# Performance work log

Hardware: AMD Instinct MI355X
Metric: run time of the kernel (lower is better)

Reference implementation:

```python
import jax, jax.numpy as jnp
import numpy as np

CUTOFF_UPPER = 4.5
EYE3 = jnp.eye(3, dtype=jnp.float32)


def tensor_norm(t):
    return (t ** 2).sum((-2, -1))


def decompose_tensor(X):
    # X: [N, C, 3, 3]
    tr_mean = jnp.trace(X, axis1=-2, axis2=-1) / 3.0
    I = tr_mean[..., None, None] * EYE3
    Xt = jnp.swapaxes(X, -2, -1)
    A = 0.5 * (X - Xt)
    S = 0.5 * (X + Xt) - I
    return I, A, S


def chan_linear(T, W, b):
    # torch: Linear applied over the channel axis after permute(0,2,3,1)
    # T: [N, C, 3, 3], W: [C, C], b: [C]
    return jnp.einsum('nkij,ck->ncij', T, W) + b[None, :, None, None]


def setup_inputs() -> dict:
    key = jax.random.key(0)
    ks = jax.random.split(key, 16)
    Np1, H, R, E = 20001, 128, 64, 200000
    X = jax.random.normal(ks[0], (Np1, H, 3, 3), dtype=jnp.float32)
    edge_index = jax.random.randint(ks[1], (2, E), 0, Np1)
    edge_weight = jax.random.uniform(ks[2], (E,), dtype=jnp.float32) * CUTOFF_UPPER
    edge_attr = jax.random.normal(ks[3], (E, R), dtype=jnp.float32)
    s = lambda fin: 1.0 / np.sqrt(fin)
    W1 = jax.random.uniform(ks[4], (3, H, H), minval=-s(H), maxval=s(H), dtype=jnp.float32)
    b1 = jax.random.uniform(ks[5], (3, H), minval=-s(H), maxval=s(H), dtype=jnp.float32)
    W2a = jax.random.uniform(ks[6], (H, R), minval=-s(R), maxval=s(R), dtype=jnp.float32)
    b2a = jax.random.uniform(ks[7], (H,), minval=-s(R), maxval=s(R), dtype=jnp.float32)
    W2b = jax.random.uniform(ks[8], (2 * H, H), minval=-s(H), maxval=s(H), dtype=jnp.float32)
    b2b = jax.random.uniform(ks[9], (2 * H,), minval=-s(H), maxval=s(H), dtype=jnp.float32)
    W2c = jax.random.uniform(ks[10], (3 * H, 2 * H), minval=-s(2 * H), maxval=s(2 * H), dtype=jnp.float32)
    b2c = jax.random.uniform(ks[11], (3 * H,), minval=-s(2 * H), maxval=s(2 * H), dtype=jnp.float32)
    W3 = jax.random.uniform(ks[12], (3, H, H), minval=-s(H), maxval=s(H), dtype=jnp.float32)
    b3 = jax.random.uniform(ks[13], (3, H), minval=-s(H), maxval=s(H), dtype=jnp.float32)
    return dict(X=X, edge_index=edge_index, edge_weight=edge_weight, edge_attr=edge_attr,
                W1=W1, b1=b1, W2a=W2a, b2a=b2a, W2b=W2b, b2b=b2b, W2c=W2c, b2c=b2c, W3=W3, b3=b3)


def reference(X, edge_index, edge_weight, edge_attr, W1, b1, W2a, b2a, W2b, b2b, W2c, b2c, W3, b3):
    Np1, H = X.shape[0], X.shape[1]
    act = jax.nn.silu
    X = X / (tensor_norm(X) + 1.0)[..., None, None]
    I, A, S = decompose_tensor(X)
    I = chan_linear(I, W1[0], b1[0])
    A = chan_linear(A, W1[1], b1[1])
    S = chan_linear(S, W1[2], b1[2])
    Y = I + A + S
    h = act(edge_attr @ W2a.T + b2a)
    h = act(h @ W2b.T + b2b)
    h = act(h @ W2c.T + b2c)  # [E, 3H]
    C = 0.5 * (jnp.cos(edge_weight * (jnp.pi / CUTOFF_UPPER)) + 1.0)
    C = C * (edge_weight < CUTOFF_UPPER).astype(C.dtype)
    ea = (h * C[:, None]).reshape(h.shape[0], H, 3)
    dst, src = edge_index[0], edge_index[1]

    def mp(factor, T):
        msg = factor[:, :, None, None] * T[src]  # [E, H, 3, 3]
        return jax.ops.segment_sum(msg, dst, num_segments=Np1)

    msg = mp(ea[..., 0], I) + mp(ea[..., 1], A) + mp(ea[..., 2], S)
    new_features = jnp.matmul(msg, Y) + jnp.matmul(Y, msg)  # O(3) branch
    I, A, S = decompose_tensor(new_features)
    norm = (tensor_norm(I + A + S) + 1.0)[..., None, None]
    I, A, S = I / norm, A / norm, S / norm
    I = chan_linear(I, W3[0], b3[0])
    A = chan_linear(A, W3[1], b3[1])
    S = chan_linear(S, W3[2], b3[2])
    dX = I + A + S
    return X + dX + jnp.matmul(dX, dX)
```

## Files before the change

kernel.cpp:

```cpp
#include <hip/hip_runtime.h>
#include <math.h>
#include <stdint.h>

typedef unsigned short u16;
typedef __attribute__((ext_vector_type(8))) short short8;
typedef __attribute__((ext_vector_type(4))) float floatx4;

__device__ __forceinline__ float b2f(u16 u){
  union{unsigned int i; float f;} v; v.i = ((unsigned int)u)<<16; return v.f;
}
__device__ __forceinline__ u16 f2b(float f){
  union{unsigned int i; float f;} v; v.f = f;
  unsigned int r = (v.i + 0x7FFFu + ((v.i>>16)&1u))>>16;
  return (u16)r;
}
__device__ __forceinline__ unsigned int pu(u16 lo, u16 hi){
  return (unsigned int)lo | ((unsigned int)hi<<16);
}
__device__ __forceinline__ float gsel(unsigned int u, int s){
  return b2f((u16)(s ? (u>>16) : (u & 0xffffu)));
}
__device__ __forceinline__ unsigned int cvtpk(float a, float b){
  unsigned int r;
  asm("v_cvt_pk_bf16_f32 %0, %1, %2" : "=v"(r) : "v"(a), "v"(b));
  return r;
}
__device__ __forceinline__ float fsilu(float t){
  float e = __builtin_amdgcn_exp2f(t * -1.442695040888963f);
  return t * __builtin_amdgcn_rcpf(1.0f + e);
}
__device__ __forceinline__ float ldx(const void* p, size_t i, int isb){
  return isb ? b2f(((const u16*)p)[i]) : ((const float*)p)[i];
}
__device__ __forceinline__ void gll16(const u16* g, u16* l){
  __builtin_amdgcn_global_load_lds(
      (const __attribute__((address_space(1))) unsigned int*)(g),
      (__attribute__((address_space(3))) unsigned int*)(l), 16, 0, 0);
}

__global__ void k_sniff(const void* __restrict__ X, int* __restrict__ flag)
{
  __shared__ int cnt;
  if (threadIdx.x==0) cnt = 0;
  __syncthreads();
  int c = 0;
  for (int t = threadIdx.x; t < 512; t += 256){
    unsigned int u = ((const u16*)X)[2*t];
    int e = (u >> 7) & 0xFF;
    if (e >= 110 && e <= 139) c++;
  }
  atomicAdd(&cnt, c);
  __syncthreads();
  if (threadIdx.x==0) *flag = (cnt > 300) ? 1 : 0;
}

__global__ __launch_bounds__(256) void k_zero_int(int* __restrict__ p, int n)
{
  int i = blockIdx.x*256 + threadIdx.x;
  if (i < n) p[i] = 0;
}

__global__ __launch_bounds__(256) void k_hist(
    const int* __restrict__ ei, int* __restrict__ counts, int E)
{
  int e = blockIdx.x*256 + threadIdx.x;
  if (e < E) atomicAdd(&counts[ei[e]], 1);
}
__global__ __launch_bounds__(256) void k_scan(
    const int* __restrict__ counts, int* __restrict__ rowptr,
    int* __restrict__ fill, int N)
{
  __shared__ int sm[256];
  int tid = threadIdx.x;
  int per = (N + 255) >> 8;
  int lo = tid*per; if (lo > N) lo = N;
  int hi = lo + per; if (hi > N) hi = N;
  int s = 0;
  for (int i = lo; i < hi; i++) s += counts[i];
  sm[tid] = s;
  __syncthreads();
  for (int off=1; off<256; off<<=1){
    int t = (tid >= off) ? sm[tid-off] : 0;
    __syncthreads();
    sm[tid] += t;
    __syncthreads();
  }
  int run = sm[tid] - s;
  for (int i = lo; i < hi; i++){
    int v = counts[i];
    rowptr[i] = run; fill[i] = run;
    run += v;
  }
  if (tid == 0) rowptr[N] = sm[255];
}
__global__ __launch_bounds__(256) void k_scatter(
    const int* __restrict__ ei, int* __restrict__ fill,
    int* __restrict__ eorder, int E)
{
  int e = blockIdx.x*256 + threadIdx.x;
  if (e >= E) return;
  int d = ei[e];
  int pos = atomicAdd(&fill[d], 1);
  eorder[pos] = e;
}

__global__ __launch_bounds__(256) void k_cvt_weights(
    const void* __restrict__ W1, const void* __restrict__ W3,
    const void* __restrict__ W2a, const void* __restrict__ W2b,
    const void* __restrict__ W2c, u16* __restrict__ out,
    const int* __restrict__ dflag)
{
  int isb = *dflag;
  int i = blockIdx.x*256 + threadIdx.x;
  if (i >= 237568) return;
  float v;
  if (i < 49152)        v = ldx(W1, i, isb);
  else if (i < 98304)   v = ldx(W3, i-49152, isb);
  else if (i < 106496)  v = ldx(W2a, i-98304, isb);
  else if (i < 139264)  v = ldx(W2b, i-106496, isb);
  else {
    int j = i - 139264;
    int r = j >> 8, c = j & 255;
    v = ldx(W2c, (size_t)((r & 127)*3 + (r >> 7))*256 + c, isb);
  }
  out[i] = f2b(v);
}
__global__ __launch_bounds__(256) void k_cvt_biases(
    const void* __restrict__ b2a, const void* __restrict__ b2b,
    const void* __restrict__ b2c, float* __restrict__ out,
    const int* __restrict__ dflag)
{
  int isb = *dflag;
  int i = blockIdx.x*256 + threadIdx.x;
  if (i < 128) out[i] = ldx(b2a, i, isb);
  else if (i < 384) out[i] = ldx(b2b, i-128, isb);
  else if (i < 768){ int c = i-384; out[i] = ldx(b2c, (c&127)*3 + (c>>7), isb); }
}
__global__ __launch_bounds__(256) void k_perm_eatt(
    const void* __restrict__ eatt, const int* __restrict__ eorder,
    u16* __restrict__ dst, int E, const int* __restrict__ dflag)
{
  int isb = *dflag;
  int row = blockIdx.x*8 + (threadIdx.x >> 5);
  int cp = (threadIdx.x & 31)*2;
  if (row >= E) return;
  int e = eorder[row];
  unsigned int w;
  if (isb){
    w = *(const unsigned int*)((const u16*)eatt + (size_t)e*64 + cp);
  } else {
    float2 v = *(const float2*)((const float*)eatt + (size_t)e*64 + cp);
    w = pu(f2b(v.x), f2b(v.y));
  }
  *(unsigned int*)(dst + (size_t)row*64 + cp) = w;
}

__global__ __launch_bounds__(256) void k_decompose(
    const void* __restrict__ X, u16* __restrict__ Di, u16* __restrict__ Da,
    u16* __restrict__ Ds, int NH, const int* __restrict__ dflag)
{
  __shared__ __align__(16) float buf[4608];
  u16* bufu = (u16*)buf;
  int isb = *dflag;
  int tid = threadIdx.x;
  size_t t0 = (size_t)blockIdx.x*512;
  int validT = (int)((size_t)NH - t0); if (validT > 512) validT = 512;
  int ve = validT*9;
  if (isb){
    const u16* src = (const u16*)X + t0*9;
    for (int idx = tid; idx*8 < ve; idx += 256){
      if (idx*8+7 < ve) ((uint4*)bufu)[idx] = *(const uint4*)(src + idx*8);
      else for (int j=idx*8; j<ve; j++) bufu[j] = src[j];
    }
  } else {
    const float* src = (const float*)X + t0*9;
    for (int idx = tid; idx*4 < ve; idx += 256){
      if (idx*4+3 < ve) ((float4*)buf)[idx] = *(const float4*)(src + idx*4);
      else for (int j=idx*4; j<ve; j++) buf[j] = src[j];
    }
  }
  __syncthreads();
  int pairs = validT >> 1;
  if (tid >= pairs) return;
  int l2 = 2*tid;
  size_t tid2 = t0 + l2;
  int n = (int)(tid2 >> 7), c = (int)(tid2 & 127);
  u16 ri[2], ra[2][3], rs[2][6];
#pragma unroll
  for (int s=0; s<2; s++){
    float x[9]; float nrm = 0.f;
#pragma unroll
    for (int i=0;i<9;i++){
      x[i] = isb ? b2f(bufu[(l2+s)*9+i]) : buf[(l2+s)*9+i];
      nrm += x[i]*x[i];
    }
    float inv = 1.0f/(nrm+1.0f);
#pragma unroll
    for (int i=0;i<9;i++) x[i]*=inv;
    float i0 = (x[0]+x[4]+x[8])*(1.0f/3.0f);
    ri[s] = f2b(i0);
    ra[s][0] = f2b(0.5f*(x[1]-x[3]));
    ra[s][1] = f2b(0.5f*(x[2]-x[6]));
    ra[s][2] = f2b(0.5f*(x[5]-x[7]));
    rs[s][0] = f2b(x[0]-i0);
    rs[s][1] = f2b(0.5f*(x[1]+x[3]));
    rs[s][2] = f2b(0.5f*(x[2]+x[6]));
    rs[s][3] = f2b(x[4]-i0);
    rs[s][4] = f2b(0.5f*(x[5]+x[7]));
    rs[s][5] = f2b(x[8]-i0);
  }
  *(unsigned int*)&Di[tid2] = pu(ri[0], ri[1]);
  size_t ab = ((size_t)n*3)*128 + c;
#pragma unroll
  for (int j=0;j<3;j++)
    *(unsigned int*)&Da[ab + (size_t)j*128] = pu(ra[0][j], ra[1][j]);
  size_t sb = ((size_t)n*6)*128 + c;
#pragma unroll
  for (int j=0;j<6;j++)
    *(unsigned int*)&Ds[sb + (size_t)j*128] = pu(rs[0][j], rs[1][j]);
}

__global__ __launch_bounds__(256) void k_mfma_gemm(
    const u16* __restrict__ A, const u16* __restrict__ B,
    const float* __restrict__ bias, const float* __restrict__ rowscale,
    u16* __restrict__ C, int M, int Ncol, int K, int flags)
{
  __shared__ u16 As[4096];
  __shared__ u16 Bs[4096];
  const int tid = threadIdx.x;
  const int lane = tid & 63, l15 = lane & 15, q = lane >> 4;
  const int wid = tid >> 6, wm = wid & 1, wn = wid >> 1;
  const int n0 = blockIdx.x * 128, m0 = blockIdx.y * 128;

  const int srow = wid*32 + (lane >> 2);
  const int qsrc = (lane & 3) ^ ((lane >> 3) & 3);
  int ar0 = m0 + srow;      if (ar0 >= M) ar0 = M-1;
  int ar1 = m0 + srow + 16; if (ar1 >= M) ar1 = M-1;
  const u16* aSrc0 = A + (size_t)ar0*K + qsrc*8;
  const u16* aSrc1 = A + (size_t)ar1*K + qsrc*8;
  const u16* bSrc0 = B + (size_t)(n0 + srow)*K + qsrc*8;
  const u16* bSrc1 = B + (size_t)(n0 + srow + 16)*K + qsrc*8;
  u16* aDst0 = &As[wid*1024];  u16* aDst1 = &As[wid*1024 + 512];
  u16* bDst0 = &Bs[wid*1024];  u16* bDst1 = &Bs[wid*1024 + 512];

  floatx4 acc[4][4];
#pragma unroll
  for (int i=0;i<4;i++)
#pragma unroll
    for (int j=0;j<4;j++) acc[i][j] = (floatx4)0.f;

  const int qsw  = ((q ^ ((l15 >> 1) & 3)) << 3);
  const int aBase = (wm*64 + l15)*32 + qsw;
  const int bBase = (wn*64 + l15)*32 + qsw;

  for (int k0 = 0; k0 < K; k0 += 32){
    gll16(aSrc0 + k0, aDst0);
    gll16(aSrc1 + k0, aDst1);
    gll16(bSrc0 + k0, bDst0);
    gll16(bSrc1 + k0, bDst1);
    __syncthreads();
    short8 av[4], bv[4];
#pragma unroll
    for (int mt=0; mt<4; mt++)
      av[mt] = *reinterpret_cast<const short8*>(&As[aBase + mt*512]);
#pragma unroll
    for (int nt=0; nt<4; nt++)
      bv[nt] = *reinterpret_cast<const short8*>(&Bs[bBase + nt*512]);
#pragma unroll
    for (int mt=0; mt<4; mt++)
#pragma unroll
      for (int nt=0; nt<4; nt++)
        acc[mt][nt] = __builtin_amdgcn_mfma_f32_16x16x32_bf16(av[mt], bv[nt], acc[mt][nt], 0, 0, 0);
    __syncthreads();
  }

  float biasv[4];
#pragma unroll
  for (int nt=0; nt<4; nt++)
    biasv[nt] = bias ? bias[n0 + wn*64 + nt*16 + l15] : 0.f;
#pragma unroll
  for (int mt=0; mt<4; mt++){
#pragma unroll
    for (int reg=0; reg<4; reg++){
      int row = m0 + wm*64 + mt*16 + q*4 + reg;
      if (row >= M) continue;
      float rs = (flags & 2) ? rowscale[row] : 1.0f;
      float t[4];
#pragma unroll
      for (int nt=0; nt<4; nt++){
        float v = acc[mt][nt][reg] + biasv[nt];
        if (flags & 1) v = fsilu(v);
        t[nt] = v * rs;
      }
      unsigned int p0 = cvtpk(t[0], t[1]);
      unsigned int p1 = cvtpk(t[2], t[3]);
      size_t rb = (size_t)row*Ncol + n0 + wn*64 + l15;
      C[rb]      = (u16)(p0 & 0xffffu);
      C[rb + 16] = (u16)(p0 >> 16);
      C[rb + 32] = (u16)(p1 & 0xffffu);
      C[rb + 48] = (u16)(p1 >> 16);
    }
  }
}

__global__ __launch_bounds__(256) void k_cutoff(
    const void* __restrict__ ew, const int* __restrict__ eorder, int c0,
    float* __restrict__ Cc, int ec, const int* __restrict__ dflag)
{
  int i = blockIdx.x*256 + threadIdx.x;
  if (i >= ec) return;
  int e = eorder[c0 + i];
  float w = ldx(ew, e, *dflag);
  float c = 0.0f;
  if (w < 4.5f) c = 0.5f*(cosf(w*0.6981317007977318f) + 1.0f);
  Cc[i] = c;
}

__global__ __launch_bounds__(128) void k_gather(
    const int* __restrict__ rowptr, const int* __restrict__ eorder,
    const int* __restrict__ ei, int E, int c0, int c1, int first,
    const u16* __restrict__ ea,
    const u16* __restrict__ Pi, const u16* __restrict__ Pa,
    const u16* __restrict__ Ps, const void* __restrict__ b1,
    float* __restrict__ msg, int NH, const int* __restrict__ dflag)
{
  int n = blockIdx.x;
  int lo = rowptr[n], hi = rowptr[n+1];
  if (lo < c0) lo = c0;
  if (hi > c1) hi = c1;
  if (!first && lo >= hi) return;
  int isb = *dflag;
  int c = threadIdx.x;
  float m[9];
#pragma unroll
  for (int i=0;i<9;i++) m[i]=0.f;
  if (lo < hi){
    float b0 = ldx(b1,c,isb), b1f = ldx(b1,128+c,isb), b2v = ldx(b1,256+c,isb);
    for (int idx = lo; idx < hi; idx++){
      int e = eorder[idx];
      int src = ei[E + e];
      const u16* er = ea + (size_t)(idx - c0)*384;
      float e0f = b2f(er[c]), e1f = b2f(er[128+c]), e2f = b2f(er[256+c]);
      float i1 = b2f(Pi[(size_t)src*128 + c]);
      size_t ab = (size_t)src*384 + c;
      float a0 = b2f(Pa[ab]), a1 = b2f(Pa[ab+128]), a2 = b2f(Pa[ab+256]);
      size_t sb = (size_t)src*768 + c;
      float s0 = b2f(Ps[sb]),     s1 = b2f(Ps[sb+128]), s2 = b2f(Ps[sb+256]);
      float s3 = b2f(Ps[sb+384]), s4 = b2f(Ps[sb+512]), s5 = b2f(Ps[sb+640]);
      float bb = e0f*b0 + e1f*b1f + e2f*b2v;
      float t0 = e0f*i1;
      m[0] += t0 + e2f*s0 + bb;
      m[1] += e1f*a0 + e2f*s1 + bb;
      m[2] += e1f*a1 + e2f*s2 + bb;
      m[3] += -e1f*a0 + e2f*s1 + bb;
      m[4] += t0 + e2f*s3 + bb;
      m[5] += e1f*a2 + e2f*s4 + bb;
      m[6] += -e1f*a1 + e2f*s2 + bb;
      m[7] += -e1f*a2 + e2f*s4 + bb;
      m[8] += t0 + e2f*s5 + bb;
    }
  }
  size_t o = (size_t)n*128 + c;
  if (first){
#pragma unroll
    for (int i=0;i<9;i++) msg[(size_t)i*NH + o] = m[i];
  } else {
#pragma unroll
    for (int i=0;i<9;i++) msg[(size_t)i*NH + o] += m[i];
  }
}

__global__ __launch_bounds__(256) void k_update(
    const float* __restrict__ msg, const u16* __restrict__ Pi,
    const u16* __restrict__ Pa, const u16* __restrict__ Ps,
    const void* __restrict__ b1,
    u16* __restrict__ D2i, u16* __restrict__ D2a, u16* __restrict__ D2s,
    int NH, const int* __restrict__ dflag)
{
  size_t tid2 = ((size_t)blockIdx.x*256 + threadIdx.x)*2;
  if (tid2 >= (size_t)NH) return;
  int isb = *dflag;
  int n = (int)(tid2 >> 7), c = (int)(tid2 & 127);
  float Mx[2][9];
#pragma unroll
  for (int i=0;i<9;i++){
    float2 v = *(const float2*)&msg[(size_t)i*NH + tid2];
    Mx[0][i] = v.x; Mx[1][i] = v.y;
  }
  unsigned int ui = *(const unsigned int*)&Pi[tid2];
  size_t ab = ((size_t)n*3)*128 + c;
  unsigned int ua[3];
#pragma unroll
  for (int j=0;j<3;j++) ua[j] = *(const unsigned int*)&Pa[ab + (size_t)j*128];
  size_t sb = ((size_t)n*6)*128 + c;
  unsigned int us[6];
#pragma unroll
  for (int j=0;j<6;j++) us[j] = *(const unsigned int*)&Ps[sb + (size_t)j*128];
  u16 ri[2], ra[2][3], rs[2][6];
#pragma unroll
  for (int s=0; s<2; s++){
    float i1 = gsel(ui,s);
    float a0 = gsel(ua[0],s), a1 = gsel(ua[1],s), a2 = gsel(ua[2],s);
    float s0 = gsel(us[0],s), s1 = gsel(us[1],s), s2 = gsel(us[2],s);
    float s3 = gsel(us[3],s), s4 = gsel(us[4],s), s5 = gsel(us[5],s);
    float B = ldx(b1,c+s,isb) + ldx(b1,128+c+s,isb) + ldx(b1,256+c+s,isb);
    float Y[9];
    Y[0]= i1+s0+B; Y[1]= a0+s1+B; Y[2]= a1+s2+B;
    Y[3]=-a0+s1+B; Y[4]= i1+s3+B; Y[5]= a2+s4+B;
    Y[6]=-a1+s2+B; Y[7]=-a2+s4+B; Y[8]= i1+s5+B;
    float F[9];
#pragma unroll
    for (int i=0;i<3;i++)
#pragma unroll
      for (int j=0;j<3;j++){
        float acc = 0.f;
#pragma unroll
        for (int t=0;t<3;t++)
          acc += Mx[s][i*3+t]*Y[t*3+j] + Y[i*3+t]*Mx[s][t*3+j];
        F[i*3+j] = acc;
      }
    float nrm = 0.f;
#pragma unroll
    for (int i=0;i<9;i++) nrm += F[i]*F[i];
    float inv = 1.0f/(nrm+1.0f);
    float i2 = (F[0]+F[4]+F[8])*(1.0f/3.0f);
    ri[s] = f2b(i2*inv);
    ra[s][0] = f2b(0.5f*(F[1]-F[3])*inv);
    ra[s][1] = f2b(0.5f*(F[2]-F[6])*inv);
    ra[s][2] = f2b(0.5f*(F[5]-F[7])*inv);
    rs[s][0] = f2b((F[0]-i2)*inv);
    rs[s][1] = f2b(0.5f*(F[1]+F[3])*inv);
    rs[s][2] = f2b(0.5f*(F[2]+F[6])*inv);
    rs[s][3] = f2b((F[4]-i2)*inv);
    rs[s][4] = f2b(0.5f*(F[5]+F[7])*inv);
    rs[s][5] = f2b((F[8]-i2)*inv);
  }
  *(unsigned int*)&D2i[tid2] = pu(ri[0], ri[1]);
#pragma unroll
  for (int j=0;j<3;j++)
    *(unsigned int*)&D2a[ab + (size_t)j*128] = pu(ra[0][j], ra[1][j]);
#pragma unroll
  for (int j=0;j<6;j++)
    *(unsigned int*)&D2s[sb + (size_t)j*128] = pu(rs[0][j], rs[1][j]);
}

__global__ __launch_bounds__(256) void k_final(
    const void* __restrict__ X, const u16* __restrict__ P2i,
    const u16* __restrict__ P2a, const u16* __restrict__ P2s,
    const void* __restrict__ b3, void* __restrict__ out, int NH,
    const int* __restrict__ dflag)
{
  __shared__ __align__(16) float buf[4608];
  u16* bufu = (u16*)buf;
  int isb = *dflag;
  int tid = threadIdx.x;
  size_t t0 = (size_t)blockIdx.x*512;
  int validT = (int)((size_t)NH - t0); if (validT > 512) validT = 512;
  int ve = validT*9;
  if (isb){
    const u16* src = (const u16*)X + t0*9;
    for (int idx = tid; idx*8 < ve; idx += 256){
      if (idx*8+7 < ve) ((uint4*)bufu)[idx] = *(const uint4*)(src + idx*8);
      else for (int j=idx*8; j<ve; j++) bufu[j] = src[j];
    }
  } else {
    const float* src = (const float*)X + t0*9;
    for (int idx = tid; idx*4 < ve; idx += 256){
      if (idx*4+3 < ve) ((float4*)buf)[idx] = *(const float4*)(src + idx*4);
      else for (int j=idx*4; j<ve; j++) buf[j] = src[j];
    }
  }
  __syncthreads();
  int pairs = validT >> 1;
  int l2 = 2*tid;
  size_t tid2 = t0 + l2;
  float vout[2][9];
  if (tid < pairs){
    int n = (int)(tid2 >> 7), c = (int)(tid2 & 127);
    unsigned int ui = *(const unsigned int*)&P2i[tid2];
    size_t ab = ((size_t)n*3)*128 + c;
    unsigned int ua[3];
#pragma unroll
    for (int j=0;j<3;j++) ua[j] = *(const unsigned int*)&P2a[ab + (size_t)j*128];
    size_t sb = ((size_t)n*6)*128 + c;
    unsigned int us[6];
#pragma unroll
    for (int j=0;j<6;j++) us[j] = *(const unsigned int*)&P2s[sb + (size_t)j*128];
#pragma unroll
    for (int s=0; s<2; s++){
      float i1 = gsel(ui,s);
      float a0 = gsel(ua[0],s), a1 = gsel(ua[1],s), a2 = gsel(ua[2],s);
      float s0 = gsel(us[0],s), s1 = gsel(us[1],s), s2 = gsel(us[2],s);
      float s3 = gsel(us[3],s), s4 = gsel(us[4],s), s5 = gsel(us[5],s);
      float B = ldx(b3,c+s,isb) + ldx(b3,128+c+s,isb) + ldx(b3,256+c+s,isb);
      float dX[9];
      dX[0]= i1+s0+B; dX[1]= a0+s1+B; dX[2]= a1+s2+B;
      dX[3]=-a0+s1+B; dX[4]= i1+s3+B; dX[5]= a2+s4+B;
      dX[6]=-a1+s2+B; dX[7]=-a2+s4+B; dX[8]= i1+s5+B;
      float x[9]; float nrm = 0.f;
#pragma unroll
      for (int i=0;i<9;i++){
        x[i] = isb ? b2f(bufu[(l2+s)*9+i]) : buf[(l2+s)*9+i];
        nrm += x[i]*x[i];
      }
      float inv = 1.0f/(nrm+1.0f);
#pragma unroll
      for (int i=0;i<3;i++)
#pragma unroll
        for (int j=0;j<3;j++){
          float acc = 0.f;
#pragma unroll
          for (int t=0;t<3;t++) acc += dX[i*3+t]*dX[t*3+j];
          vout[s][i*3+j] = x[i*3+j]*inv + dX[i*3+j] + acc;
        }
    }
  }
  __syncthreads();
  if (tid < pairs){
    if (isb){
#pragma unroll
      for (int s=0;s<2;s++)
#pragma unroll
        for (int i=0;i<9;i++) bufu[(l2+s)*9+i] = f2b(vout[s][i]);
    } else {
#pragma unroll
      for (int s=0;s<2;s++)
#pragma unroll
        for (int i=0;i<9;i++) buf[(l2+s)*9+i] = vout[s][i];
    }
  }
  __syncthreads();
  if (isb){
    u16* dst = (u16*)out + t0*9;
    for (int idx = tid; idx*8 < ve; idx += 256){
      if (idx*8+7 < ve) *(uint4*)(dst + idx*8) = ((const uint4*)bufu)[idx];
      else for (int j=idx*8; j<ve; j++) dst[j] = bufu[j];
    }
  } else {
    float* dst = (float*)out + t0*9;
    for (int idx = tid; idx*4 < ve; idx += 256){
      if (idx*4+3 < ve) *(float4*)(dst + idx*4) = ((const float4*)buf)[idx];
      else for (int j=idx*4; j<ve; j++) dst[j] = buf[j];
    }
  }
}

extern "C" void kernel_launch(void* const* d_in, const int* in_sizes, int n_in,
                              void* d_out, int out_size, void* d_ws, size_t ws_size,
                              hipStream_t stream)
{
  const void* X    = d_in[0];
  const int*  ei   = (const int*)d_in[1];
  const void* ew   = d_in[2];
  const void* eatt = d_in[3];
  const void* W1   = d_in[4];
  const void* b1   = d_in[5];
  const void* W2a  = d_in[6];
  const void* b2a  = d_in[7];
  const void* W2b  = d_in[8];
  const void* b2b  = d_in[9];
  const void* W2c  = d_in[10];
  const void* b2c  = d_in[11];
  const void* W3   = d_in[12];
  const void* b3   = d_in[13];

  const int NH = in_sizes[0]/9;
  const int E  = in_sizes[2];
  const int N  = NH/128;

  auto aln = [](size_t x){ return (x + 255) & ~(size_t)255; };
  char* ws = (char*)d_ws;
  size_t off = 0;
  size_t o_flag = off; off += 256;
  size_t o_msg  = off; off += aln((size_t)NH*9*4);
  size_t o_Di   = off; off += aln((size_t)NH*2);
  size_t o_Da   = off; off += aln((size_t)NH*6);
  size_t o_Ds   = off; off += aln((size_t)NH*12);
  size_t o_Pi   = off; off += aln((size_t)NH*2);
  size_t o_Pa   = off; off += aln((size_t)NH*6);
  size_t o_Ps   = off; off += aln((size_t)NH*12);
  size_t o_cnt  = off; off += aln((size_t)N*4);
  size_t o_rp   = off; off += aln((size_t)(N+1)*4);
  size_t o_fill = off; off += aln((size_t)N*4);
  size_t o_eord = off; off += aln((size_t)E*4);
  size_t o_eattb= off; off += aln((size_t)E*64*2);
  size_t o_wb   = off; off += aln((size_t)237568*2);
  size_t o_bf   = off; off += aln((size_t)768*4);
  size_t persistent = off;

  int EC;
  {
    size_t avail = (ws_size > persistent + 4096) ? (ws_size - persistent - 4096) : 0;
    size_t ecmax = avail / 1540;
    if (ecmax > (size_t)E) ecmax = (size_t)E;
    EC = (int)(ecmax & ~(size_t)1023);
    if (EC < 1024) EC = 1024;
  }
  size_t o_h1 = persistent;
  size_t o_h2 = o_h1 + aln((size_t)EC*256);
  size_t o_ea = o_h2 + aln((size_t)EC*512);
  size_t o_Cc = o_ea + aln((size_t)EC*768);
  (void)n_in; (void)out_size;

  int* dflag = (int*)(ws + o_flag);
  u16* Di = (u16*)(ws + o_Di);
  u16* Da = (u16*)(ws + o_Da);
  u16* Ds = (u16*)(ws + o_Ds);
  u16* Pi = (u16*)(ws + o_Pi);
  u16* Pa = (u16*)(ws + o_Pa);
  u16* Ps = (u16*)(ws + o_Ps);
  float* msg = (float*)(ws + o_msg);
  int* counts = (int*)(ws + o_cnt);
  int* rowptr = (int*)(ws + o_rp);
  int* fill   = (int*)(ws + o_fill);
  int* eorder = (int*)(ws + o_eord);
  u16* eattb  = (u16*)(ws + o_eattb);
  u16* wb     = (u16*)(ws + o_wb);
  float* bf   = (float*)(ws + o_bf);
  u16* h1 = (u16*)(ws + o_h1);
  u16* h2 = (u16*)(ws + o_h2);
  u16* ea = (u16*)(ws + o_ea);
  float* Cc = (float*)(ws + o_Cc);

  dim3 blk(256);
  auto gemm = [&](const u16* A, const u16* Bw, const float* bias, const float* rs,
                  u16* C, int M, int Ncol, int K, int flags){
    dim3 grid(Ncol/128, (M+127)/128);
    k_mfma_gemm<<<grid, blk, 0, stream>>>(A, Bw, bias, rs, C, M, Ncol, K, flags);
  };

  k_sniff<<<1, blk, 0, stream>>>(X, dflag);
  k_cvt_weights<<<(237568+255)/256, blk, 0, stream>>>(W1, W3, W2a, W2b, W2c, wb, dflag);
  k_cvt_biases<<<3, blk, 0, stream>>>(b2a, b2b, b2c, bf, dflag);
  k_decompose<<<(NH+511)/512, blk, 0, stream>>>(X, Di, Da, Ds, NH, dflag);
  gemm(Di, wb,       nullptr, nullptr, Pi, N,   128, 128, 0);
  gemm(Da, wb+16384, nullptr, nullptr, Pa, 3*N, 128, 128, 0);
  gemm(Ds, wb+32768, nullptr, nullptr, Ps, 6*N, 128, 128, 0);
  k_zero_int<<<(N+255)/256, blk, 0, stream>>>(counts, N);
  k_hist<<<(E+255)/256, blk, 0, stream>>>(ei, counts, E);
  k_scan<<<1, blk, 0, stream>>>(counts, rowptr, fill, N);
  k_scatter<<<(E+255)/256, blk, 0, stream>>>(ei, fill, eorder, E);
  k_perm_eatt<<<(E+7)/8, blk, 0, stream>>>(eatt, eorder, eattb, E, dflag);
  for (int c0 = 0; c0 < E; c0 += EC){
    int ec = E - c0; if (ec > EC) ec = EC;
    k_cutoff<<<(ec+255)/256, blk, 0, stream>>>(ew, eorder, c0, Cc, ec, dflag);
    gemm(eattb + (size_t)c0*64, wb+98304,  bf,     nullptr, h1, ec, 128, 64,  1);
    gemm(h1,                    wb+106496, bf+128, nullptr, h2, ec, 256, 128, 1);
    gemm(h2,                    wb+139264, bf+384, Cc,      ea, ec, 384, 256, 1|2);
    k_gather<<<N, dim3(128), 0, stream>>>(rowptr, eorder, ei, E, c0, c0+ec,
                                          (c0==0)?1:0,
                                          ea, Pi, Pa, Ps, b1, msg, NH, dflag);
  }
  k_update<<<(NH/2+255)/256, blk, 0, stream>>>(msg, Pi, Pa, Ps, b1, Di, Da, Ds, NH, dflag);
  gemm(Di, wb+49152, nullptr, nullptr, Pi, N,   128, 128, 0);
  gemm(Da, wb+65536, nullptr, nullptr, Pa, 3*N, 128, 128, 0);
  gemm(Ds, wb+81920, nullptr, nullptr, Ps, 6*N, 128, 128, 0);
  k_final<<<(NH+511)/512, blk, 0, stream>>>(X, Pi, Pa, Ps, b3, d_out, NH, dflag);
}
```

Measured before the change: 840.0 us.

## Precompute sorted source indices and vectorize gather over channel pairs and edge slots

```diff
diff --git a/kernel.cpp b/kernel.cpp
--- a/kernel.cpp
+++ b/kernel.cpp
@@ -18,7 +18,9 @@
   return (unsigned int)lo | ((unsigned int)hi<<16);
 }
 __device__ __forceinline__ float gsel(unsigned int u, int s){
-  return b2f((u16)(s ? (u>>16) : (u & 0xffffu)));
+  union{unsigned int i; float f;} v;
+  v.i = s ? (u & 0xffff0000u) : (u << 16);
+  return v.f;
 }
 __device__ __forceinline__ unsigned int cvtpk(float a, float b){
   unsigned int r;
@@ -95,13 +97,14 @@
 }
 __global__ __launch_bounds__(256) void k_scatter(
     const int* __restrict__ ei, int* __restrict__ fill,
-    int* __restrict__ eorder, int E)
+    int* __restrict__ eorder, int* __restrict__ srcs, int E)
 {
   int e = blockIdx.x*256 + threadIdx.x;
   if (e >= E) return;
   int d = ei[e];
   int pos = atomicAdd(&fill[d], 1);
   eorder[pos] = e;
+  srcs[pos] = ei[E + e];
 }
 
 __global__ __launch_bounds__(256) void k_cvt_weights(
@@ -317,8 +320,8 @@
 }
 
 __global__ __launch_bounds__(128) void k_gather(
-    const int* __restrict__ rowptr, const int* __restrict__ eorder,
-    const int* __restrict__ ei, int E, int c0, int c1, int first,
+    const int* __restrict__ rowptr, const int* __restrict__ srcs,
+    int c0, int c1, int first,
     const u16* __restrict__ ea,
     const u16* __restrict__ Pi, const u16* __restrict__ Pa,
     const u16* __restrict__ Ps, const void* __restrict__ b1,
@@ -329,44 +332,92 @@
   if (lo < c0) lo = c0;
   if (hi > c1) hi = c1;
   if (!first && lo >= hi) return;
-  int isb = *dflag;
-  int c = threadIdx.x;
-  float m[9];
-#pragma unroll
-  for (int i=0;i<9;i++) m[i]=0.f;
+  int tid = threadIdx.x;
+  int slot = tid >> 6;
+  int cp = (tid & 63) * 2;
+  float m[2][9];
+#pragma unroll
+  for (int s=0;s<2;s++)
+#pragma unroll
+    for (int i=0;i<9;i++) m[s][i]=0.f;
   if (lo < hi){
-    float b0 = ldx(b1,c,isb), b1f = ldx(b1,128+c,isb), b2v = ldx(b1,256+c,isb);
-    for (int idx = lo; idx < hi; idx++){
-      int e = eorder[idx];
-      int src = ei[E + e];
+    int isb = *dflag;
+    float b0[2], b1v[2], b2v[2];
+#pragma unroll
+    for (int s=0;s<2;s++){
+      b0[s]  = ldx(b1, cp+s,     isb);
+      b1v[s] = ldx(b1, 128+cp+s, isb);
+      b2v[s] = ldx(b1, 256+cp+s, isb);
+    }
+    for (int idx = lo + slot; idx < hi; idx += 2){
+      int src = srcs[idx];
       const u16* er = ea + (size_t)(idx - c0)*384;
-      float e0f = b2f(er[c]), e1f = b2f(er[128+c]), e2f = b2f(er[256+c]);
-      float i1 = b2f(Pi[(size_t)src*128 + c]);
-      size_t ab = (size_t)src*384 + c;
-      float a0 = b2f(Pa[ab]), a1 = b2f(Pa[ab+128]), a2 = b2f(Pa[ab+256]);
-      size_t sb = (size_t)src*768 + c;
-      float s0 = b2f(Ps[sb]),     s1 = b2f(Ps[sb+128]), s2 = b2f(Ps[sb+256]);
-      float s3 = b2f(Ps[sb+384]), s4 = b2f(Ps[sb+512]), s5 = b2f(Ps[sb+640]);
-      float bb = e0f*b0 + e1f*b1f + e2f*b2v;
-      float t0 = e0f*i1;
-      m[0] += t0 + e2f*s0 + bb;
-      m[1] += e1f*a0 + e2f*s1 + bb;
-      m[2] += e1f*a1 + e2f*s2 + bb;
-      m[3] += -e1f*a0 + e2f*s1 + bb;
-      m[4] += t0 + e2f*s3 + bb;
-      m[5] += e1f*a2 + e2f*s4 + bb;
-      m[6] += -e1f*a1 + e2f*s2 + bb;
-      m[7] += -e1f*a2 + e2f*s4 + bb;
-      m[8] += t0 + e2f*s5 + bb;
-    }
-  }
-  size_t o = (size_t)n*128 + c;
-  if (first){
-#pragma unroll
-    for (int i=0;i<9;i++) msg[(size_t)i*NH + o] = m[i];
-  } else {
-#pragma unroll
-    for (int i=0;i<9;i++) msg[(size_t)i*NH + o] += m[i];
+      unsigned int ue0 = *(const unsigned int*)(er + cp);
+      unsigned int ue1 = *(const unsigned int*)(er + 128 + cp);
+      unsigned int ue2 = *(const unsigned int*)(er + 256 + cp);
+      unsigned int upi = *(const unsigned int*)(Pi + (size_t)src*128 + cp);
+      size_t ab = (size_t)src*384 + cp;
+      unsigned int ua0 = *(const unsigned int*)(Pa + ab);
+      unsigned int ua1 = *(const unsigned int*)(Pa + ab + 128);
+      unsigned int ua2 = *(const unsigned int*)(Pa + ab + 256);
+      size_t sbb = (size_t)src*768 + cp;
+      unsigned int us0 = *(const unsigned int*)(Ps + sbb);
+      unsigned int us1 = *(const unsigned int*)(Ps + sbb + 128);
+      unsigned int us2 = *(const unsigned int*)(Ps + sbb + 256);
+      unsigned int us3 = *(const unsigned int*)(Ps + sbb + 384);
+      unsigned int us4 = *(const unsigned int*)(Ps + sbb + 512);
+      unsigned int us5 = *(const unsigned int*)(Ps + sbb + 640);
+#pragma unroll
+      for (int s=0;s<2;s++){
+        float e0f = gsel(ue0,s), e1f = gsel(ue1,s), e2f = gsel(ue2,s);
+        float i1 = gsel(upi,s);
+        float a0 = gsel(ua0,s), a1 = gsel(ua1,s), a2 = gsel(ua2,s);
+        float s0 = gsel(us0,s), s1 = gsel(us1,s), s2 = gsel(us2,s);
+        float s3 = gsel(us3,s), s4 = gsel(us4,s), s5 = gsel(us5,s);
+        float bb = e0f*b0[s] + e1f*b1v[s] + e2f*b2v[s];
+        float t0 = e0f*i1;
+        m[s][0] += t0 + e2f*s0 + bb;
+        m[s][1] += e1f*a0 + e2f*s1 + bb;
+        m[s][2] += e1f*a1 + e2f*s2 + bb;
+        m[s][3] += -e1f*a0 + e2f*s1 + bb;
+        m[s][4] += t0 + e2f*s3 + bb;
+        m[s][5] += e1f*a2 + e2f*s4 + bb;
+        m[s][6] += -e1f*a1 + e2f*s2 + bb;
+        m[s][7] += -e1f*a2 + e2f*s4 + bb;
+        m[s][8] += t0 + e2f*s5 + bb;
+      }
+    }
+  }
+  __shared__ float red[64][18];
+  if (slot == 1){
+#pragma unroll
+    for (int s=0;s<2;s++)
+#pragma unroll
+      for (int i=0;i<9;i++) red[tid & 63][s*9+i] = m[s][i];
+  }
+  __syncthreads();
+  if (slot == 0){
+    int cl = tid & 63;
+#pragma unroll
+    for (int s=0;s<2;s++)
+#pragma unroll
+      for (int i=0;i<9;i++) m[s][i] += red[cl][s*9+i];
+    size_t o = (size_t)n*128 + cp;
+    if (first){
+#pragma unroll
+      for (int i=0;i<9;i++){
+        float2 v = {m[0][i], m[1][i]};
+        *(float2*)&msg[(size_t)i*NH + o] = v;
+      }
+    } else {
+#pragma unroll
+      for (int i=0;i<9;i++){
+        float2* p = (float2*)&msg[(size_t)i*NH + o];
+        float2 v = *p;
+        v.x += m[0][i]; v.y += m[1][i];
+        *p = v;
+      }
+    }
   }
 }
 
@@ -583,6 +634,7 @@
   size_t o_rp   = off; off += aln((size_t)(N+1)*4);
   size_t o_fill = off; off += aln((size_t)N*4);
   size_t o_eord = off; off += aln((size_t)E*4);
+  size_t o_srcs = off; off += aln((size_t)E*4);
   size_t o_eattb= off; off += aln((size_t)E*64*2);
   size_t o_wb   = off; off += aln((size_t)237568*2);
   size_t o_bf   = off; off += aln((size_t)768*4);
@@ -614,6 +666,7 @@
   int* rowptr = (int*)(ws + o_rp);
   int* fill   = (int*)(ws + o_fill);
   int* eorder = (int*)(ws + o_eord);
+  int* srcs   = (int*)(ws + o_srcs);
   u16* eattb  = (u16*)(ws + o_eattb);
   u16* wb     = (u16*)(ws + o_wb);
   float* bf   = (float*)(ws + o_bf);
@@ -639,7 +692,7 @@
   k_zero_int<<<(N+255)/256, blk, 0, stream>>>(counts, N);
   k_hist<<<(E+255)/256, blk, 0, stream>>>(ei, counts, E);
   k_scan<<<1, blk, 0, stream>>>(counts, rowptr, fill, N);
-  k_scatter<<<(E+255)/256, blk, 0, stream>>>(ei, fill, eorder, E);
+  k_scatter<<<(E+255)/256, blk, 0, stream>>>(ei, fill, eorder, srcs, E);
   k_perm_eatt<<<(E+7)/8, blk, 0, stream>>>(eatt, eorder, eattb, E, dflag);
   for (int c0 = 0; c0 < E; c0 += EC){
     int ec = E - c0; if (ec > EC) ec = EC;
@@ -647,7 +700,7 @@
     gemm(eattb + (size_t)c0*64, wb+98304,  bf,     nullptr, h1, ec, 128, 64,  1);
     gemm(h1,                    wb+106496, bf+128, nullptr, h2, ec, 256, 128, 1);
     gemm(h2,                    wb+139264, bf+384, Cc,      ea, ec, 384, 256, 1|2);
-    k_gather<<<N, dim3(128), 0, stream>>>(rowptr, eorder, ei, E, c0, c0+ec,
+    k_gather<<<N, dim3(128), 0, stream>>>(rowptr, srcs, c0, c0+ec,
                                           (c0==0)?1:0,
                                           ea, Pi, Pa, Ps, b1, msg, NH, dflag);
   }
```

Result: no change. 829.9 us (-1.2%).
